# Kernel tuning notes

Hardware: AMD Instinct MI355X
Metric: run time of the kernel (lower is better)

Reference implementation:

```python
import jax, jax.numpy as jnp
import numpy as np

B, N, R, S, FIN, NCLS, KNN = 16, 2048, 64, 64, 6, 40, 40


def _knn_laplacian(x, k):
    # pairwise squared distance -> gaussian affinity -> row-wise top-k sparsify
    # -> symmetric-normalized Laplacian  L = I - D^{-1/2} A D^{-1/2}
    xx = jnp.sum(x * x, axis=-1)                      # [B,N]
    inner = jnp.einsum('bnd,bmd->bnm', x, x)          # [B,N,N]
    dist = xx[:, :, None] + xx[:, None, :] - 2.0 * inner
    A = jnp.exp(-dist)
    kth = jax.lax.top_k(A, k)[0][..., -1]             # k-th largest per row [B,N]
    A = jnp.where(A >= kth[..., None], A, jnp.zeros((), A.dtype))
    d = jnp.sum(A, axis=-1)
    dis = jnp.where(d > 0, jax.lax.rsqrt(jnp.maximum(d, 1e-12)), jnp.zeros((), A.dtype))
    L = jnp.eye(A.shape[-1], dtype=A.dtype) - dis[:, :, None] * A * dis[:, None, :]
    return L


def _cheb_conv(x, L, w, b):
    # DenseChebConv, K=3: T0=x, T1=Lx, T2=2LT1-T0, then linear on concat
    t0 = x
    t1 = jnp.matmul(L, x)
    t2 = 2.0 * jnp.matmul(L, t1) - t0
    xc = jnp.concatenate([t0, t1, t2], axis=-1)       # [B,N,3*Fin]
    return jnp.matmul(xc, w) + b


def setup_inputs() -> dict:
    key = jax.random.key(0)
    ks = jax.random.split(key, 16)
    p = lambda k_, sh: (jax.random.normal(k_, sh, dtype=jnp.float32) * 0.02)
    return {
        'x': jax.random.normal(ks[0], (B, N, FIN), dtype=jnp.float32),
        'laplacian_Reeb': jax.random.normal(ks[1], (B, R, R), dtype=jnp.float32),
        'sccs': jax.random.randint(ks[2], (B, R, S), 0, N),
        'vertices_reeb': jax.random.normal(ks[3], (B * R, 3), dtype=jnp.float32),
        'edges_reeb': jax.random.randint(ks[4], (B, 128, 2), 0, R),
        'labels': jax.random.randint(ks[5], (B,), 0, NCLS),
        'k': KNN, 'batch_size': B, 'num_points': N,
        'conv1_w': p(ks[6], (3 * FIN, 128)), 'conv1_b': jnp.zeros((128,), jnp.float32),
        'conv2_w': p(ks[7], (3 * 128, 512)), 'conv2_b': jnp.zeros((512,), jnp.float32),
        'convReeb_w': p(ks[8], (3 * 128, 512)), 'convReeb_b': jnp.zeros((512,), jnp.float32),
        'fc1_w': p(ks[9], (1024, 512)), 'fc1_b': jnp.zeros((512,), jnp.float32),
        'fc2_w': p(ks[10], (512, 128)), 'fc2_b': jnp.zeros((128,), jnp.float32),
        'fc3_w': p(ks[11], (128, NCLS)), 'fc3_b': jnp.zeros((NCLS,), jnp.float32),
    }


def reference(x, laplacian_Reeb, sccs, vertices_reeb, edges_reeb, labels, k,
              batch_size, num_points, conv1_w, conv1_b, conv2_w, conv2_b,
              convReeb_w, convReeb_b, fc1_w, fc1_b, fc2_w, fc2_b, fc3_w, fc3_b):
    regs = []
    # graph build is under no_grad in the original
    L = jax.lax.stop_gradient(_knn_laplacian(x, k))
    out = jax.nn.relu(_cheb_conv(x, L, conv1_w, conv1_b))           # [B,N,128]
    regs.append(jnp.linalg.norm(jnp.einsum('bnf,bnm,bmg->bfg', out, L, out)) ** 2)

    # Reeb ragged segment-max pool (no_grad in original): gather SCC index
    # groups per Reeb node and max-reduce -> [B,R,128]
    gathered = jax.vmap(lambda o, s: o[s])(out, sccs)               # [B,R,S,128]
    Vertices_final_Reeb = jax.lax.stop_gradient(jnp.max(gathered, axis=2))
    laplacian_Reeb_final = jax.lax.stop_gradient(laplacian_Reeb)

    L2 = jax.lax.stop_gradient(_knn_laplacian(out, k))
    out = jax.nn.relu(_cheb_conv(out, L2, conv2_w, conv2_b))        # [B,N,512]
    regs.append(jnp.linalg.norm(jnp.einsum('bnf,bnm,bmg->bfg', out, L2, out)) ** 2)

    out_Reeb = jax.nn.relu(_cheb_conv(Vertices_final_Reeb, laplacian_Reeb_final,
                                      convReeb_w, convReeb_b))      # [B,R,512]
    regs.append(jnp.linalg.norm(jnp.einsum('brf,brq,bqg->bfg', out_Reeb,
                                           laplacian_Reeb_final, out_Reeb)) ** 2)

    out = jnp.max(out, axis=1)            # [B,512]
    out_Reeb = jnp.max(out_Reeb, axis=1)  # [B,512]
    out = jnp.concatenate([out_Reeb, out], axis=1)                  # [B,1024]

    out = jnp.matmul(out, fc1_w) + fc1_b
    regs.append(jnp.linalg.norm(fc1_w[:, 0]) ** 2); regs.append(fc1_b[0] ** 2)
    out = jax.nn.relu(out)
    out = jnp.matmul(out, fc2_w) + fc2_b
    regs.append(jnp.linalg.norm(fc2_w[:, 0]) ** 2); regs.append(fc2_b[0] ** 2)
    out = jax.nn.relu(out)
    out = jnp.matmul(out, fc3_w) + fc3_b
    regs.append(jnp.linalg.norm(fc3_w[:, 0]) ** 2); regs.append(fc3_b[0] ** 2)
    return out, jnp.stack(regs)
```

## Files before the change

### kernel.cpp

```cpp
#include <hip/hip_runtime.h>

#define NB 16
#define NP 2048
#define NR 64
#define NS 64
#define KSEL 40

typedef __attribute__((ext_vector_type(8))) short bf16x8;
typedef __attribute__((ext_vector_type(4))) float f32x4;

constexpr long aOUT1 = 0;
constexpr long aT1A  = aOUT1 + 16L*2048*128;
constexpr long aT2A  = aT1A  + 16L*2048*6;
constexpr long aZ1   = aT2A  + 16L*2048*6;
constexpr long aM1   = aZ1   + 16L*2048*128;
constexpr long aVALS1= aM1   + 16L*128*128;
constexpr long aDIS1 = aVALS1+ 16L*2048*64;
constexpr long aVALS2= aDIS1 + 16L*2048;
constexpr long aDIS2 = aVALS2+ 16L*2048*64;
constexpr long aXX2  = aDIS2 + 16L*2048;
constexpr long aXX1  = aXX2  + 16L*2048;
constexpr long aG4   = aXX1  + 16L*2048;
constexpr long aT1B  = aG4   + 4L*2048*2048;
constexpr long aT2B  = aT1B  + 16L*2048*128;
constexpr long aOUT2 = aT2B  + 16L*2048*128;
constexpr long aZ2   = aOUT2 + 16L*2048*512;
constexpr long aM2   = aZ2   + 16L*2048*512;
constexpr long aVFR  = aM2   + 16L*512*512;
constexpr long aT1R  = aVFR  + 16L*64*128;
constexpr long aT2R  = aT1R  + 16L*64*128;
constexpr long aOUTR = aT2R  + 16L*64*128;
constexpr long aZR   = aOUTR + 16L*64*512;
constexpr long aMR   = aZR   + 16L*64*512;
constexpr long aPOOL = aMR   + 16L*512*512;
constexpr long aFC1O = aPOOL + 16L*1024;
constexpr long aFC2O = aFC1O + 16L*512;
constexpr long aMPP  = aFC2O + 16L*128;
constexpr long FTOT  = aMPP  + 16L*8*512;

constexpr long iCOLS1 = 0;
constexpr long iCNT1  = iCOLS1 + 16L*2048*64;
constexpr long iCOLS2 = iCNT1  + 16L*2048;
constexpr long iCNT2  = iCOLS2 + 16L*2048*64;
constexpr long ITOT   = iCNT2  + 16L*2048;

constexpr long uOUT1H = 0;
constexpr long uOUT1L = uOUT1H + 16L*2048*128;
constexpr long uT1BH  = uOUT1L + 16L*2048*128;
constexpr long uT1BL  = uT1BH  + 16L*2048*128;
constexpr long uT2BH  = uT1BL  + 16L*2048*128;
constexpr long uT2BL  = uT2BH  + 16L*2048*128;
constexpr long uW2TH  = uT2BL  + 16L*2048*128;
constexpr long uW2TL  = uW2TH  + 512L*384;
constexpr long uVFRH  = uW2TL  + 512L*384;
constexpr long uVFRL  = uVFRH  + 16L*64*128;
constexpr long uT1RH  = uVFRL  + 16L*64*128;
constexpr long uT1RL  = uT1RH  + 16L*64*128;
constexpr long uT2RH  = uT1RL  + 16L*64*128;
constexpr long uT2RL  = uT2RH  + 16L*64*128;
constexpr long uWRTH  = uT2RL  + 16L*64*128;
constexpr long uWRTL  = uWRTH  + 512L*384;
constexpr long uOUT1T = uWRTL  + 512L*384;
constexpr long uZ1T   = uOUT1T + 16L*128*2048;
constexpr long uOUT2T = uZ1T   + 16L*128*2048;
constexpr long uZ2T   = uOUT2T + 16L*512*2048;
constexpr long uOUTRT = uZ2T   + 16L*512*2048;
constexpr long uZRT   = uOUTRT + 16L*512*64;
constexpr long uOUT2B = uZRT   + 16L*512*64;
constexpr long UTOT   = uOUT2B + 16L*2048*512;

__device__ __align__(256) float  g_farena[FTOT];
__device__ __align__(256) int    g_iarena[ITOT];
__device__ __align__(256) ushort g_uarena[UTOT];

__device__ __forceinline__ float wsum_f(float v){
  #pragma unroll
  for (int s=32;s>0;s>>=1) v += __shfl_xor(v, s, 64);
  return v;
}
__device__ __forceinline__ int wsum_i(int v){
  #pragma unroll
  for (int s=32;s>0;s>>=1) v += __shfl_xor(v, s, 64);
  return v;
}

__device__ __forceinline__ void gl2lds16(const void* g, void* l){
  __builtin_amdgcn_global_load_lds(
      (const __attribute__((address_space(1))) void*)g,
      (__attribute__((address_space(3))) void*)l, 16, 0, 0);
}

__device__ __forceinline__ unsigned fkey(float f){
  unsigned b = __float_as_uint(f);
  return b ^ (((unsigned)((int)b >> 31)) | 0x80000000u);
}
__device__ __forceinline__ float fkey_inv(unsigned k){
  unsigned m = ((unsigned)((int)(~k) >> 31)) | 0x80000000u;
  return __uint_as_float(k ^ m);
}

__device__ __forceinline__ void topk_store(unsigned (&uk)[32], int lane, long row,
    int* __restrict__ cols, float* __restrict__ vals,
    int* __restrict__ cnt, float* __restrict__ dis)
{
  unsigned kmax = uk[0], kmin = uk[0];
  #pragma unroll
  for (int q=1;q<32;++q){
    kmax = kmax > uk[q] ? kmax : uk[q];
    kmin = kmin < uk[q] ? kmin : uk[q];
  }
  #pragma unroll
  for (int s=32;s>0;s>>=1){
    unsigned o1 = (unsigned)__shfl_xor((int)kmax, s, 64);
    unsigned o2 = (unsigned)__shfl_xor((int)kmin, s, 64);
    kmax = kmax > o1 ? kmax : o1;
    kmin = kmin < o2 ? kmin : o2;
  }
  unsigned lo = kmin, hi = kmax + 1u;
  int cLo = 2048, cHi = 0, it = 0;
  while (cLo != KSEL && hi - lo > 1u){
    unsigned t;
    if (it & 1){
      t = lo + ((hi - lo) >> 1);
    } else {
      float flo = fkey_inv(lo), fhi = fkey_inv(hi);
      float ft = flo + (fhi - flo) * ((float)(cLo - KSEL) / (float)(cLo - cHi));
      t = fkey(ft);
      if (t <= lo) t = lo + 1u;
      else if (t >= hi) t = hi - 1u;
    }
    ++it;
    int c = 0;
    #pragma unroll
    for (int q=0;q<32;++q) c += (int)__popcll(__ballot(uk[q] >= t));
    if (c >= KSEL){ lo = t; cLo = c; } else { hi = t; cHi = c; }
  }
  unsigned kth = lo;
  int kc = 0;
  #pragma unroll
  for (int q=0;q<32;++q) kc += (uk[q] >= kth) ? 1 : 0;
  int tot = wsum_i(kc);
  int incl = kc;
  #pragma unroll
  for (int s=1;s<64;s<<=1){ int u = __shfl_up(incl, s, 64); if (lane >= s) incl += u; }
  int pos = incl - kc;
  int* cp = cols + row*64; float* vp = vals + row*64;
  float d = 0.f;
  #pragma unroll
  for (int q=0;q<32;++q){
    if (uk[q] >= kth){
      float v = __expf(fkey_inv(uk[q]));
      d += v;
      if (pos < 64){ cp[pos] = q*64 + lane; vp[pos] = v; }
      pos++;
    }
  }
  d = wsum_f(d);
  if (lane == 0){
    cnt[row] = tot <= 64 ? tot : 64;
    dis[row] = d > 0.f ? (1.0f / sqrtf(fmaxf(d, 1e-12f))) : 0.f;
  }
}

__global__ __launch_bounds__(256) void xx6_kernel(const float* __restrict__ x,
    float* __restrict__ xx1)
{
  long i = (long)blockIdx.x*256 + threadIdx.x;
  const float* p = x + i*6;
  float2 v0 = *(const float2*)(p);
  float2 v1 = *(const float2*)(p+2);
  float2 v2 = *(const float2*)(p+4);
  xx1[i] = v0.x*v0.x + v0.y*v0.y + v1.x*v1.x + v1.y*v1.y + v2.x*v2.x + v2.y*v2.y;
}

__global__ __launch_bounds__(256) void knn1_kernel(const float* __restrict__ x,
    const float* __restrict__ xx1,
    int* __restrict__ cols, float* __restrict__ vals, int* __restrict__ cnt,
    float* __restrict__ dis)
{
  int lane = threadIdx.x & 63;
  long row = (long)blockIdx.x*4 + (threadIdx.x >> 6);
  int b = (int)(row >> 11); int i = (int)(row & (NP-1));
  const float* xb = x + (long)b*NP*6;
  const float* xxb = xx1 + ((long)b << 11);
  float xi[6];
  #pragma unroll
  for (int d2=0; d2<6; ++d2) xi[d2] = xb[(long)i*6 + d2];
  float xxi = xxb[i];
  unsigned uk[32];
  #pragma unroll 4
  for (int c=0;c<32;++c){
    int j = c*64 + lane;
    const float* xj = xb + (long)j*6;
    float2 v0 = *(const float2*)(xj);
    float2 v1 = *(const float2*)(xj+2);
    float2 v2 = *(const float2*)(xj+4);
    float inr = xi[0]*v0.x + xi[1]*v0.y + xi[2]*v1.x + xi[3]*v1.y + xi[4]*v2.x + xi[5]*v2.y;
    uk[c] = fkey(2.f*inr - xxi - xxb[j]);
  }
  topk_store(uk, lane, row, cols, vals, cnt, dis);
}

__global__ __launch_bounds__(256) void knn2_kernel(const float* __restrict__ G,
    const float* __restrict__ xx, int batch0,
    int* __restrict__ cols, float* __restrict__ vals, int* __restrict__ cnt,
    float* __restrict__ dis)
{
  int lane = threadIdx.x & 63;
  long lrow = (long)blockIdx.x*4 + (threadIdx.x >> 6);
  int lb = (int)(lrow >> 11); int i = (int)(lrow & (NP-1));
  long row = ((long)(batch0+lb) << 11) + i;
  const float* Gr = G + ((long)lb*NP + i)*NP;
  const float* xxb = xx + ((long)(batch0+lb) << 11);
  float xxi = xxb[i];
  unsigned uk[32];
  #pragma unroll 4
  for (int c=0;c<32;++c){
    int j = c*64 + lane;
    uk[c] = fkey(2.f*Gr[j] - xxi - xxb[j]);
  }
  topk_store(uk, lane, row, cols, vals, cnt, dis);
}

__global__ __launch_bounds__(256) void spmm6_kernel(const float* __restrict__ X,
    const float* __restrict__ T0, float* __restrict__ Y,
    const int* __restrict__ cols, const float* __restrict__ vals,
    const int* __restrict__ cnt, const float* __restrict__ dis,
    float c1, float c2, float cs)
{
  long row = (long)blockIdx.x*256 + threadIdx.x;
  int b = (int)(row >> 11);
  const float* Xb = X + ((long)b << 11)*6;
  const float* db = dis + ((long)b << 11);
  float acc[6] = {0,0,0,0,0,0};
  int c = cnt[row];
  const int* cp = cols + row*64; const float* vp = vals + row*64;
  for (int t=0;t<c;++t){
    int j = cp[t];
    float w = vp[t] * db[j];
    const float* xr = Xb + (long)j*6;
    #pragma unroll
    for (int d2=0; d2<6; ++d2) acc[d2] += w * xr[d2];
  }
  float di = dis[row];
  #pragma unroll
  for (int d2=0; d2<6; ++d2)
    Y[row*6+d2] = c1*X[row*6+d2] + c2*T0[row*6+d2] - cs*di*acc[d2];
}

template<int W>
__global__ __launch_bounds__((W >= 256) ? 256 : W) void spmm_kernel(
    const float* __restrict__ X, const float* __restrict__ T0, float* __restrict__ Y,
    const int* __restrict__ cols, const float* __restrict__ vals,
    const int* __restrict__ cnt, const float* __restrict__ dis,
    float c1, float c2, float cs)
{
  constexpr int TPB = (W >= 256) ? 256 : W;
  constexpr int E = W / TPB;
  __shared__ int scol[64];
  __shared__ float sval[64];
  int q = blockIdx.x;
  long row = ((long)(q & 7) << 12) + (q >> 3);
  int b = (int)(row >> 11);
  int tid = threadIdx.x;
  int c = cnt[row];
  if (tid < 64){ scol[tid] = cols[row*64+tid]; sval[tid] = vals[row*64+tid]; }
  __syncthreads();
  const float* Xb = X + ((long)b << 11)*W;
  const float* db = dis + ((long)b << 11);
  float acc[E] = {};
  for (int t=0;t<c;++t){
    int j = scol[t];
    float w = sval[t] * db[j];
    const float* xr = Xb + (long)j*W;
    #pragma unroll
    for (int e=0;e<E;++e) acc[e] += w * xr[tid + e*TPB];
  }
  float di = dis[row];
  #pragma unroll
  for (int e=0;e<E;++e){
    long idx = row*W + tid + e*TPB;
    Y[idx] = c1*X[idx] + c2*T0[idx] - cs*di*acc[e];
  }
}

__global__ __launch_bounds__(256) void spmmb_kernel(
    const float* __restrict__ X, const ushort* __restrict__ Xb,
    float* __restrict__ Y,
    const int* __restrict__ cols, const float* __restrict__ vals,
    const int* __restrict__ cnt, const float* __restrict__ dis)
{
  __shared__ int scol[4][64];
  __shared__ float sval[4][64];
  int q = blockIdx.x;
  int wid = threadIdx.x >> 6, lane = threadIdx.x & 63;
  long row = ((long)(q & 7) << 12) + ((long)(q >> 3) << 2) + wid;
  int b = (int)(row >> 11);
  scol[wid][lane] = cols[row*64 + lane];
  sval[wid][lane] = vals[row*64 + lane];
  const ushort* Xbb = Xb + ((long)b << 11)*512;
  const float* db = dis + ((long)b << 11);
  int c = cnt[row];
  float acc[8] = {};
  for (int t=0;t<c;++t){
    int j = scol[wid][t];
    float w = sval[wid][t] * db[j];
    bf16x8 v = *(const bf16x8*)(Xbb + (long)j*512 + lane*8);
    #pragma unroll
    for (int e=0;e<8;++e)
      acc[e] += w * __uint_as_float(((unsigned)(ushort)v[e]) << 16);
  }
  float di = dis[row];
  long base = row*512 + lane*8;
  float4 x0 = *(const float4*)(X + base);
  float4 x1 = *(const float4*)(X + base + 4);
  float4 o0, o1;
  o0.x = x0.x - di*acc[0]; o0.y = x0.y - di*acc[1];
  o0.z = x0.z - di*acc[2]; o0.w = x0.w - di*acc[3];
  o1.x = x1.x - di*acc[4]; o1.y = x1.y - di*acc[5];
  o1.z = x1.z - di*acc[6]; o1.w = x1.w - di*acc[7];
  *(float4*)(Y + base) = o0;
  *(float4*)(Y + base + 4) = o1;
}

__global__ __launch_bounds__(128) void conv1_kernel(const float* __restrict__ x,
    const float* __restrict__ t1, const float* __restrict__ t2,
    const float* __restrict__ w, const float* __restrict__ bias,
    float* __restrict__ out)
{
  long row = blockIdx.x; int o = threadIdx.x;
  float acc = bias[o];
  const float* xr = x + row*6; const float* a1 = t1 + row*6; const float* a2 = t2 + row*6;
  #pragma unroll
  for (int d2=0; d2<6; ++d2){
    acc += xr[d2]*w[d2*128 + o];
    acc += a1[d2]*w[(6+d2)*128 + o];
    acc += a2[d2]*w[(12+d2)*128 + o];
  }
  out[row*128 + o] = fmaxf(acc, 0.f);
}

__global__ __launch_bounds__(256) void pack_hilo_kernel(const float* __restrict__ X,
    ushort* __restrict__ H, ushort* __restrict__ L, long n4)
{
  long i = (long)blockIdx.x*256 + threadIdx.x;
  if (i >= n4) return;
  float4 v = *(const float4*)(X + i*4);
  float xs[4] = {v.x, v.y, v.z, v.w};
  ushort h[4], l[4];
  #pragma unroll
  for (int q=0;q<4;++q){
    unsigned u = __float_as_uint(xs[q]);
    h[q] = (ushort)(u >> 16);
    float hf = __uint_as_float(u & 0xffff0000u);
    float r = xs[q] - hf;
    l[q] = (ushort)(__float_as_uint(r) >> 16);
  }
  *(ushort4*)(H + i*4) = make_ushort4(h[0],h[1],h[2],h[3]);
  *(ushort4*)(L + i*4) = make_ushort4(l[0],l[1],l[2],l[3]);
}

__global__ __launch_bounds__(256) void pack_rne_kernel(const float* __restrict__ X,
    ushort* __restrict__ H, long n4)
{
  long i = (long)blockIdx.x*256 + threadIdx.x;
  if (i >= n4) return;
  float4 v = *(const float4*)(X + i*4);
  float xs[4] = {v.x, v.y, v.z, v.w};
  ushort h[4];
  #pragma unroll
  for (int q=0;q<4;++q){
    unsigned u = __float_as_uint(xs[q]);
    u += 0x7fffu + ((u >> 16) & 1u);
    h[q] = (ushort)(u >> 16);
  }
  *(ushort4*)(H + i*4) = make_ushort4(h[0],h[1],h[2],h[3]);
}

template<bool HILO>
__global__ __launch_bounds__(256) void tpack_kernel(const float* __restrict__ X,
    ushort* __restrict__ H, ushort* __restrict__ L,
    int R, int C, long sIn, long sOut)
{
  __shared__ float tile[32][33];
  int c0 = blockIdx.x*32, r0 = blockIdx.y*32, b = blockIdx.z;
  const float* Xb = X + (long)b*sIn;
  int tx = threadIdx.x & 31, ty = threadIdx.x >> 5;
  #pragma unroll
  for (int rr=ty; rr<32; rr+=8)
    tile[rr][tx] = Xb[(long)(r0+rr)*C + c0+tx];
  __syncthreads();
  #pragma unroll
  for (int cc=ty; cc<32; cc+=8){
    float xv = tile[tx][cc];
    long oidx = (long)b*sOut + (long)(c0+cc)*R + r0 + tx;
    unsigned u = __float_as_uint(xv);
    if (HILO){
      H[oidx] = (ushort)(u >> 16);
      float hf = __uint_as_float(u & 0xffff0000u);
      float r = xv - hf;
      L[oidx] = (ushort)(__float_as_uint(r) >> 16);
    } else {
      u += 0x7fffu + ((u >> 16) & 1u);
      H[oidx] = (ushort)(u >> 16);
    }
  }
}

__global__ __launch_bounds__(256) void mirror_kernel(float* __restrict__ G)
{
  int p = blockIdx.y;
  int t = p, bx = 0, rem = 15;
  while (t >= rem){ t -= rem; --rem; ++bx; }
  int by = bx + 1 + t;
  int sub = blockIdx.x;
  int si = sub >> 2, sj = sub & 3;
  int r0 = bx*128 + si*32;
  int c0 = by*128 + sj*32;
  float* Gb = G + (long)blockIdx.z*NP*NP;
  __shared__ float tile[32][33];
  int tx = threadIdx.x & 31, ty = threadIdx.x >> 5;
  #pragma unroll
  for (int rr=ty; rr<32; rr+=8)
    tile[rr][tx] = Gb[(long)(r0+rr)*NP + c0+tx];
  __syncthreads();
  #pragma unroll
  for (int rr=ty; rr<32; rr+=8)
    Gb[(long)(c0+rr)*NP + r0+tx] = tile[tx][rr];
}

template<bool SPLIT, bool CHEB, bool BR, bool TRI>
__global__ __launch_bounds__(256) void mgemm_kernel(
    const ushort* __restrict__ Ah0, const ushort* __restrict__ Ah1, const ushort* __restrict__ Ah2,
    const ushort* __restrict__ Al0, const ushort* __restrict__ Al1, const ushort* __restrict__ Al2,
    const ushort* __restrict__ Bh, const ushort* __restrict__ Bl,
    const float* __restrict__ bias, float* __restrict__ C,
    int M, int N, int K, long sA, long sB, long sC)
{
  __shared__ ushort AsH[128*32];
  __shared__ ushort BsH[128*32];
  __shared__ ushort AsL[SPLIT ? 128*32 : 8];
  __shared__ ushort BsL[SPLIT ? 128*32 : 8];
  int bz = blockIdx.z;
  int m0, n0;
  if constexpr (TRI){
    int t = blockIdx.x, bx = 0, rem = 16;
    while (t >= rem){ t -= rem; --rem; ++bx; }
    m0 = bx*128; n0 = (bx + t)*128;
  } else {
    m0 = blockIdx.x*128; n0 = blockIdx.y*128;
  }
  int tid = threadIdx.x, lane = tid & 63, wid = tid >> 6;
  int wm = (wid & 1)*64, wn = (wid >> 1)*64;
  f32x4 acc[4][4] = {};
  const ushort* Bb  = Bh + (long)bz*sB;
  const ushort* Blb = SPLIT ? (Bl + (long)bz*sB) : (const ushort*)nullptr;
  const ushort* Ab  = CHEB ? Ah0 : (Ah0 + (long)bz*sA);
  const ushort* Alb = (SPLIT && !CHEB) ? (Al0 + (long)bz*sA) : Al0;

  for (int k0 = 0; k0 < K; k0 += 32){
    #pragma unroll
    for (int cc2=0; cc2<2; ++cc2){
      int chunk = wid*2 + cc2;
      int e = chunk*512 + lane*8;
      int row = e >> 5;
      int slot = (e >> 3) & 3;
      int scol = (slot ^ ((row >> 1) & 3)) * 8;
      const ushort* asrc;
      if (CHEB){
        int kg2 = k0 + scol;
        const ushort* base = (kg2 < 128) ? Ah0 : ((kg2 < 256) ? Ah1 : Ah2);
        asrc = base + (long)(m0+row)*128 + (kg2 & 127);
      } else {
        asrc = Ab + (long)(m0+row)*K + k0 + scol;
      }
      gl2lds16(asrc, &AsH[chunk*512]);
      gl2lds16(Bb + (long)(n0+row)*K + k0 + scol, &BsH[chunk*512]);
      if (SPLIT){
        const ushort* alsrc;
        if (CHEB){
          int kg2 = k0 + scol;
          const ushort* base = (kg2 < 128) ? Al0 : ((kg2 < 256) ? Al1 : Al2);
          alsrc = base + (long)(m0+row)*128 + (kg2 & 127);
        } else {
          alsrc = Alb + (long)(m0+row)*K + k0 + scol;
        }
        gl2lds16(alsrc, &AsL[chunk*512]);
        gl2lds16(Blb + (long)(n0+row)*K + k0 + scol, &BsL[chunk*512]);
      }
    }
    __syncthreads();
    int lr = lane & 15, kg = lane >> 4;
    bf16x8 af[4], bfr[4];
    #pragma unroll
    for (int f=0; f<4; ++f){
      int ra = wm + f*16 + lr;
      int rb = wn + f*16 + lr;
      af[f]  = *(const bf16x8*)&AsH[ra*32 + (kg ^ ((ra>>1)&3))*8];
      bfr[f] = *(const bf16x8*)&BsH[rb*32 + (kg ^ ((rb>>1)&3))*8];
    }
    if (SPLIT){
      bf16x8 al[4], bl[4];
      #pragma unroll
      for (int f=0; f<4; ++f){
        int ra = wm + f*16 + lr;
        int rb = wn + f*16 + lr;
        al[f] = *(const bf16x8*)&AsL[ra*32 + (kg ^ ((ra>>1)&3))*8];
        bl[f] = *(const bf16x8*)&BsL[rb*32 + (kg ^ ((rb>>1)&3))*8];
      }
      #pragma unroll
      for (int mf=0; mf<4; ++mf)
        #pragma unroll
        for (int nf=0; nf<4; ++nf){
          acc[mf][nf] = __builtin_amdgcn_mfma_f32_16x16x32_bf16(af[mf], bfr[nf], acc[mf][nf], 0,0,0);
          acc[mf][nf] = __builtin_amdgcn_mfma_f32_16x16x32_bf16(af[mf], bl[nf],  acc[mf][nf], 0,0,0);
          acc[mf][nf] = __builtin_amdgcn_mfma_f32_16x16x32_bf16(al[mf], bfr[nf], acc[mf][nf], 0,0,0);
        }
    } else {
      #pragma unroll
      for (int mf=0; mf<4; ++mf)
        #pragma unroll
        for (int nf=0; nf<4; ++nf)
          acc[mf][nf] = __builtin_amdgcn_mfma_f32_16x16x32_bf16(af[mf], bfr[nf], acc[mf][nf], 0,0,0);
    }
    __syncthreads();
  }
  int lr = lane & 15, l4 = (lane >> 4)*4;
  #pragma unroll
  for (int mf=0; mf<4; ++mf){
    #pragma unroll
    for (int nf=0; nf<4; ++nf){
      int n = n0 + wn + nf*16 + lr;
      float bv = BR ? bias[n] : 0.f;
      #pragma unroll
      for (int r=0; r<4; ++r){
        int m = m0 + wm + mf*16 + l4 + r;
        float v = acc[mf][nf][r];
        if (BR) v = fmaxf(v + bv, 0.f);
        C[(long)bz*sC + (long)m*N + n] = v;
      }
    }
  }
}

__global__ __launch_bounds__(256) void rownorm_kernel(const float* __restrict__ X,
    float* __restrict__ xx)
{
  int lane = threadIdx.x & 63;
  long row = (long)blockIdx.x*4 + (threadIdx.x >> 6);
  const float* p = X + row*128;
  float v0 = p[lane], v1 = p[64+lane];
  float s = wsum_f(v0*v0 + v1*v1);
  if (lane == 0) xx[row] = s;
}

__global__ __launch_bounds__(128) void reeb_pool_kernel(const float* __restrict__ out1,
    const int* __restrict__ sccs, float* __restrict__ VfR)
{
  int q = blockIdx.x;
  int br = ((q & 7) << 7) + (q >> 3);
  int b = br >> 6;
  int f = threadIdx.x;
  const int* sp = sccs + (long)br*NS;
  const float* ob = out1 + ((long)b << 11)*128;
  float m = -1e30f;
  for (int s=0;s<NS;++s){
    int idx = sp[s];
    m = fmaxf(m, ob[(long)idx*128 + f]);
  }
  VfR[(long)br*128 + f] = m;
}

template<int W>
__global__ __launch_bounds__((W>=256)?256:W) void reeb_mm_kernel(const float* __restrict__ L,
    const float* __restrict__ X, const float* __restrict__ T0, float* __restrict__ Y,
    float cs, float c2)
{
  constexpr int TPB = (W>=256)?256:W;
  constexpr int E = W/TPB;
  int br = blockIdx.x; int b = br >> 6; int r = br & 63;
  const float* lr = L + ((long)b*NR + r)*NR;
  const float* Xb = X + (long)b*NR*W;
  int tid = threadIdx.x;
  float acc[E] = {};
  for (int q=0;q<NR;++q){
    float w = lr[q];
    #pragma unroll
    for (int e=0;e<E;++e) acc[e] += w * Xb[(long)q*W + tid + e*TPB];
  }
  #pragma unroll
  for (int e=0;e<E;++e){
    long idx = (long)br*W + tid + e*TPB;
    Y[idx] = cs*acc[e] + c2*T0[idx];
  }
}

__global__ __launch_bounds__(512) void maxpool1_kernel(const float* __restrict__ X,
    float* __restrict__ part)
{
  int b = blockIdx.x, rc = blockIdx.y; int f = threadIdx.x;
  const float* p = X + ((long)b*2048 + (long)rc*256)*512 + f;
  float m = -1e30f;
  #pragma unroll 4
  for (int r=0;r<256;++r) m = fmaxf(m, p[(long)r*512]);
  part[((long)b*8+rc)*512 + f] = m;
}

__global__ __launch_bounds__(512) void maxpool2_kernel(const float* __restrict__ part,
    const float* __restrict__ outR, float* __restrict__ pool)
{
  int b = blockIdx.x; int f = threadIdx.x;
  const float* pp = part + (long)b*8*512 + f;
  float m = -1e30f;
  #pragma unroll
  for (int r=0;r<8;++r) m = fmaxf(m, pp[r*512]);
  pool[(long)b*1024 + 512 + f] = m;
  const float* rp = outR + (long)b*64*512 + f;
  float mr = -1e30f;
  #pragma unroll 4
  for (int r=0;r<64;++r) mr = fmaxf(mr, rp[(long)r*512]);
  pool[(long)b*1024 + f] = mr;
}

template<bool RELU>
__global__ __launch_bounds__(256) void fc_kernel(const float* __restrict__ in,
    const float* __restrict__ W, const float* __restrict__ bias,
    float* __restrict__ out, int IN, int OUT)
{
  __shared__ float red[4][64];
  int b = blockIdx.x, o0 = blockIdx.y*64;
  int tid = threadIdx.x;
  int ol = tid & 63, q = tid >> 6;
  int o = o0 + ol;
  const float* ip = in + (long)b*IN;
  float acc = 0.f;
  if (o < OUT){
    int kb = IN >> 2;
    int ks = q*kb;
    for (int i=0;i<kb;i+=8){
      #pragma unroll
      for (int u=0;u<8;++u){
        int k = ks + i + u;
        acc += ip[k]*W[(long)k*OUT + o];
      }
    }
  }
  red[q][ol] = acc;
  __syncthreads();
  if (tid < 64){
    int oo = o0 + tid;
    if (oo < OUT){
      float s = red[0][tid]+red[1][tid]+red[2][tid]+red[3][tid] + bias[oo];
      out[(long)b*OUT + oo] = RELU ? fmaxf(s, 0.f) : s;
    }
  }
}

__global__ __launch_bounds__(256) void sumsq_kernel(const float* __restrict__ X, int n,
    float* __restrict__ tgt)
{
  __shared__ float ps[4];
  int tid = threadIdx.x; int lane = tid & 63, wid = tid >> 6;
  float s = 0.f;
  for (long i = (long)blockIdx.x*256 + tid; i < n; i += (long)gridDim.x*256){
    float v = X[i]; s += v*v;
  }
  s = wsum_f(s);
  if (lane == 0) ps[wid] = s;
  __syncthreads();
  if (tid == 0) atomicAdd(tgt, ps[0]+ps[1]+ps[2]+ps[3]);
}

__global__ __launch_bounds__(256) void wreg_kernel(const float* __restrict__ w1,
    const float* __restrict__ b1, const float* __restrict__ w2, const float* __restrict__ b2,
    const float* __restrict__ w3, const float* __restrict__ b3, float* __restrict__ out9)
{
  __shared__ float ps[3][4];
  int tid = threadIdx.x, lane = tid & 63, wid = tid >> 6;
  float s1 = 0.f, s2 = 0.f, s3 = 0.f;
  for (int i=tid;i<1024;i+=256){ float v = w1[(long)i*512]; s1 += v*v; }
  for (int i=tid;i<512;i+=256){ float v = w2[(long)i*128]; s2 += v*v; }
  if (tid < 128){ float v = w3[(long)tid*40]; s3 = v*v; }
  s1 = wsum_f(s1); s2 = wsum_f(s2); s3 = wsum_f(s3);
  if (lane == 0){ ps[0][wid]=s1; ps[1][wid]=s2; ps[2][wid]=s3; }
  __syncthreads();
  if (tid == 0){
    out9[3] = ps[0][0]+ps[0][1]+ps[0][2]+ps[0][3];
    out9[4] = b1[0]*b1[0];
    out9[5] = ps[1][0]+ps[1][1]+ps[1][2]+ps[1][3];
    out9[6] = b2[0]*b2[0];
    out9[7] = ps[2][0]+ps[2][1]+ps[2][2]+ps[2][3];
    out9[8] = b3[0]*b3[0];
  }
}

extern "C" void kernel_launch(void* const* d_in, const int* in_sizes, int n_in,
                              void* d_out, int out_size, void* d_ws, size_t ws_size,
                              hipStream_t stream)
{
  (void)in_sizes; (void)n_in; (void)d_ws; (void)ws_size; (void)out_size;
  const float* x    = (const float*)d_in[0];
  const float* lapR = (const float*)d_in[1];
  const int*   sccs = (const int*)d_in[2];
  const float* w1   = (const float*)d_in[9];
  const float* b1   = (const float*)d_in[10];
  const float* w2   = (const float*)d_in[11];
  const float* b2   = (const float*)d_in[12];
  const float* wR   = (const float*)d_in[13];
  const float* bRb  = (const float*)d_in[14];
  const float* fw1  = (const float*)d_in[15];
  const float* fb1  = (const float*)d_in[16];
  const float* fw2  = (const float*)d_in[17];
  const float* fb2  = (const float*)d_in[18];
  const float* fw3  = (const float*)d_in[19];
  const float* fb3  = (const float*)d_in[20];
  float* out = (float*)d_out;

  float* Fb = nullptr; int* Ib = nullptr; ushort* Ub = nullptr;
  hipGetSymbolAddress((void**)&Fb, HIP_SYMBOL(g_farena));
  hipGetSymbolAddress((void**)&Ib, HIP_SYMBOL(g_iarena));
  hipGetSymbolAddress((void**)&Ub, HIP_SYMBOL(g_uarena));

  float* out1 = Fb + aOUT1;  float* t1a = Fb + aT1A;  float* t2a = Fb + aT2A;
  float* Z1   = Fb + aZ1;    float* M1  = Fb + aM1;
  float* vals1= Fb + aVALS1; float* dis1= Fb + aDIS1;
  float* vals2= Fb + aVALS2; float* dis2= Fb + aDIS2;
  float* xx2  = Fb + aXX2;   float* xx1 = Fb + aXX1;  float* G4  = Fb + aG4;
  float* t1b  = Fb + aT1B;   float* t2b = Fb + aT2B;
  float* out2 = Fb + aOUT2;  float* Z2  = Fb + aZ2;   float* M2 = Fb + aM2;
  float* VfR  = Fb + aVFR;   float* t1R = Fb + aT1R;  float* t2R= Fb + aT2R;
  float* outR = Fb + aOUTR;  float* ZR  = Fb + aZR;   float* MR = Fb + aMR;
  float* pool = Fb + aPOOL;  float* fc1o= Fb + aFC1O; float* fc2o=Fb + aFC2O;
  float* mpp  = Fb + aMPP;
  int* cols1 = Ib + iCOLS1; int* cnt1 = Ib + iCNT1;
  int* cols2 = Ib + iCOLS2; int* cnt2 = Ib + iCNT2;
  ushort* out1h = Ub + uOUT1H; ushort* out1l = Ub + uOUT1L;
  ushort* t1bh  = Ub + uT1BH;  ushort* t1bl  = Ub + uT1BL;
  ushort* t2bh  = Ub + uT2BH;  ushort* t2bl  = Ub + uT2BL;
  ushort* w2th  = Ub + uW2TH;  ushort* w2tl  = Ub + uW2TL;
  ushort* vfrh  = Ub + uVFRH;  ushort* vfrl  = Ub + uVFRL;
  ushort* t1rh  = Ub + uT1RH;  ushort* t1rl  = Ub + uT1RL;
  ushort* t2rh  = Ub + uT2RH;  ushort* t2rl  = Ub + uT2RL;
  ushort* wrth  = Ub + uWRTH;  ushort* wrtl  = Ub + uWRTL;
  ushort* out1t = Ub + uOUT1T; ushort* z1t   = Ub + uZ1T;
  ushort* out2t = Ub + uOUT2T; ushort* z2t   = Ub + uZ2T;
  ushort* outrt = Ub + uOUTRT; ushort* zrt   = Ub + uZRT;
  ushort* out2b = Ub + uOUT2B;

  hipMemsetAsync(out + 640, 0, 9*sizeof(float), stream);

  xx6_kernel<<<dim3(128),dim3(256),0,stream>>>(x, xx1);
  knn1_kernel<<<dim3(8192),dim3(256),0,stream>>>(x, xx1, cols1, vals1, cnt1, dis1);
  spmm6_kernel<<<dim3(128),dim3(256),0,stream>>>(x, x, t1a, cols1, vals1, cnt1, dis1, 1.f, 0.f, 1.f);
  spmm6_kernel<<<dim3(128),dim3(256),0,stream>>>(t1a, x, t2a, cols1, vals1, cnt1, dis1, 2.f, -1.f, 2.f);
  conv1_kernel<<<dim3(32768),dim3(128),0,stream>>>(x, t1a, t2a, w1, b1, out1);
  pack_hilo_kernel<<<dim3(4096),dim3(256),0,stream>>>(out1, out1h, out1l, 16L*2048*128/4);

  spmm_kernel<128><<<dim3(32768),dim3(128),0,stream>>>(out1, out1, Z1, cols1, vals1, cnt1, dis1, 1.f, 0.f, 1.f);
  tpack_kernel<false><<<dim3(4,64,16),dim3(256),0,stream>>>(out1, out1t, nullptr, 2048,128, 2048L*128, 128L*2048);
  tpack_kernel<false><<<dim3(4,64,16),dim3(256),0,stream>>>(Z1,   z1t,   nullptr, 2048,128, 2048L*128, 128L*2048);
  mgemm_kernel<false,false,false,false><<<dim3(1,1,16),dim3(256),0,stream>>>(
      out1t,nullptr,nullptr, nullptr,nullptr,nullptr, z1t,nullptr, nullptr, M1,
      128,128,2048, 128L*2048, 128L*2048, 128L*128);
  sumsq_kernel<<<dim3(512),dim3(256),0,stream>>>(M1, 16*128*128, out+640);
  reeb_pool_kernel<<<dim3(1024),dim3(128),0,stream>>>(out1, sccs, VfR);

  rownorm_kernel<<<dim3(8192),dim3(256),0,stream>>>(out1, xx2);
  for (int g=0; g<4; ++g){
    long off = (long)g*4*NP*128;
    mgemm_kernel<true,false,false,true><<<dim3(136,1,4),dim3(256),0,stream>>>(
        out1h+off,nullptr,nullptr, out1l+off,nullptr,nullptr, out1h+off, out1l+off, nullptr, G4,
        2048,2048,128, (long)NP*128, (long)NP*128, (long)NP*NP);
    mirror_kernel<<<dim3(16,120,4),dim3(256),0,stream>>>(G4);
    knn2_kernel<<<dim3(2048),dim3(256),0,stream>>>(G4, xx2, g*4, cols2, vals2, cnt2, dis2);
  }
  spmm_kernel<128><<<dim3(32768),dim3(128),0,stream>>>(out1, out1, t1b, cols2, vals2, cnt2, dis2, 1.f, 0.f, 1.f);
  spmm_kernel<128><<<dim3(32768),dim3(128),0,stream>>>(t1b, out1, t2b, cols2, vals2, cnt2, dis2, 2.f, -1.f, 2.f);
  pack_hilo_kernel<<<dim3(4096),dim3(256),0,stream>>>(t1b, t1bh, t1bl, 16L*2048*128/4);
  pack_hilo_kernel<<<dim3(4096),dim3(256),0,stream>>>(t2b, t2bh, t2bl, 16L*2048*128/4);
  tpack_kernel<true><<<dim3(16,12,1),dim3(256),0,stream>>>(w2, w2th, w2tl, 384,512, 0,0);
  mgemm_kernel<true,true,true,false><<<dim3(256,4,1),dim3(256),0,stream>>>(
      out1h,t1bh,t2bh, out1l,t1bl,t2bl, w2th, w2tl, b2, out2,
      32768,512,384, 0,0,0);
  pack_rne_kernel<<<dim3(16384),dim3(256),0,stream>>>(out2, out2b, 16L*2048*512/4);
  spmmb_kernel<<<dim3(8192),dim3(256),0,stream>>>(out2, out2b, Z2, cols2, vals2, cnt2, dis2);
  tpack_kernel<false><<<dim3(16,64,16),dim3(256),0,stream>>>(out2, out2t, nullptr, 2048,512, 2048L*512, 512L*2048);
  tpack_kernel<false><<<dim3(16,64,16),dim3(256),0,stream>>>(Z2,   z2t,   nullptr, 2048,512, 2048L*512, 512L*2048);
  mgemm_kernel<false,false,false,false><<<dim3(4,4,16),dim3(256),0,stream>>>(
      out2t,nullptr,nullptr, nullptr,nullptr,nullptr, z2t,nullptr, nullptr, M2,
      512,512,2048, 512L*2048, 512L*2048, 512L*512);
  sumsq_kernel<<<dim3(512),dim3(256),0,stream>>>(M2, 16*512*512, out+641);

  reeb_mm_kernel<128><<<dim3(1024),dim3(128),0,stream>>>(lapR, VfR, VfR, t1R, 1.f, 0.f);
  reeb_mm_kernel<128><<<dim3(1024),dim3(128),0,stream>>>(lapR, t1R, VfR, t2R, 2.f, -1.f);
  pack_hilo_kernel<<<dim3(128),dim3(256),0,stream>>>(VfR, vfrh, vfrl, 16L*64*128/4);
  pack_hilo_kernel<<<dim3(128),dim3(256),0,stream>>>(t1R, t1rh, t1rl, 16L*64*128/4);
  pack_hilo_kernel<<<dim3(128),dim3(256),0,stream>>>(t2R, t2rh, t2rl, 16L*64*128/4);
  tpack_kernel<true><<<dim3(16,12,1),dim3(256),0,stream>>>(wR, wrth, wrtl, 384,512, 0,0);
  mgemm_kernel<true,true,true,false><<<dim3(8,4,1),dim3(256),0,stream>>>(
      vfrh,t1rh,t2rh, vfrl,t1rl,t2rl, wrth, wrtl, bRb, outR,
      1024,512,384, 0,0,0);
  reeb_mm_kernel<512><<<dim3(1024),dim3(256),0,stream>>>(lapR, outR, outR, ZR, 1.f, 0.f);
  tpack_kernel<false><<<dim3(16,2,16),dim3(256),0,stream>>>(outR, outrt, nullptr, 64,512, 64L*512, 512L*64);
  tpack_kernel<false><<<dim3(16,2,16),dim3(256),0,stream>>>(ZR,   zrt,   nullptr, 64,512, 64L*512, 512L*64);
  mgemm_kernel<false,false,false,false><<<dim3(4,4,16),dim3(256),0,stream>>>(
      outrt,nullptr,nullptr, nullptr,nullptr,nullptr, zrt,nullptr, nullptr, MR,
      512,512,64, 512L*64, 512L*64, 512L*512);
  sumsq_kernel<<<dim3(512),dim3(256),0,stream>>>(MR, 16*512*512, out+642);

  maxpool1_kernel<<<dim3(16,8),dim3(512),0,stream>>>(out2, mpp);
  maxpool2_kernel<<<dim3(16),dim3(512),0,stream>>>(mpp, outR, pool);
  fc_kernel<true ><<<dim3(16,8),dim3(256),0,stream>>>(pool, fw1, fb1, fc1o, 1024, 512);
  fc_kernel<true ><<<dim3(16,2),dim3(256),0,stream>>>(fc1o, fw2, fb2, fc2o, 512, 128);
  fc_kernel<false><<<dim3(16,1),dim3(256),0,stream>>>(fc2o, fw3, fb3, out, 128, 40);
  wreg_kernel<<<dim3(1),dim3(256),0,stream>>>(fw1, fb1, fw2, fb2, fw3, fb3, out+640);
}
```

Baseline: 1.216 ms.

## Fuse bf16 packing, Gram mirroring and sum-of-squares into producer kernels

```diff
diff --git a/kernel.cpp b/kernel.cpp
--- a/kernel.cpp
+++ b/kernel.cpp
@@ -25,14 +25,12 @@
 constexpr long aT2B  = aT1B  + 16L*2048*128;
 constexpr long aOUT2 = aT2B  + 16L*2048*128;
 constexpr long aZ2   = aOUT2 + 16L*2048*512;
-constexpr long aM2   = aZ2   + 16L*2048*512;
-constexpr long aVFR  = aM2   + 16L*512*512;
+constexpr long aVFR  = aZ2   + 16L*2048*512;
 constexpr long aT1R  = aVFR  + 16L*64*128;
 constexpr long aT2R  = aT1R  + 16L*64*128;
 constexpr long aOUTR = aT2R  + 16L*64*128;
 constexpr long aZR   = aOUTR + 16L*64*512;
-constexpr long aMR   = aZR   + 16L*64*512;
-constexpr long aPOOL = aMR   + 16L*512*512;
+constexpr long aPOOL = aZR   + 16L*64*512;
 constexpr long aFC1O = aPOOL + 16L*1024;
 constexpr long aFC2O = aFC1O + 16L*512;
 constexpr long aMPP  = aFC2O + 16L*128;
@@ -46,7 +44,8 @@
 
 constexpr long uOUT1H = 0;
 constexpr long uOUT1L = uOUT1H + 16L*2048*128;
-constexpr long uT1BH  = uOUT1L + 16L*2048*128;
+constexpr long uOUT1R = uOUT1L + 16L*2048*128;
+constexpr long uT1BH  = uOUT1R + 16L*2048*128;
 constexpr long uT1BL  = uT1BH  + 16L*2048*128;
 constexpr long uT2BH  = uT1BL  + 16L*2048*128;
 constexpr long uT2BL  = uT2BH  + 16L*2048*128;
@@ -90,6 +89,18 @@
       (__attribute__((address_space(3))) void*)l, 16, 0, 0);
 }
 
+__device__ __forceinline__ ushort bf_rne(float x){
+  unsigned u = __float_as_uint(x);
+  u += 0x7fffu + ((u >> 16) & 1u);
+  return (ushort)(u >> 16);
+}
+__device__ __forceinline__ void bf_hilo(float x, ushort& h, ushort& l){
+  unsigned u = __float_as_uint(x);
+  h = (ushort)(u >> 16);
+  float hf = __uint_as_float(u & 0xffff0000u);
+  l = (ushort)(__float_as_uint(x - hf) >> 16);
+}
+
 __device__ __forceinline__ unsigned fkey(float f){
   unsigned b = __float_as_uint(f);
   return b ^ (((unsigned)((int)b >> 31)) | 0x80000000u);
@@ -248,9 +259,10 @@
     Y[row*6+d2] = c1*X[row*6+d2] + c2*T0[row*6+d2] - cs*di*acc[d2];
 }
 
-template<int W>
+template<int W, bool PACK>
 __global__ __launch_bounds__((W >= 256) ? 256 : W) void spmm_kernel(
     const float* __restrict__ X, const float* __restrict__ T0, float* __restrict__ Y,
+    ushort* __restrict__ Hh, ushort* __restrict__ Ll,
     const int* __restrict__ cols, const float* __restrict__ vals,
     const int* __restrict__ cnt, const float* __restrict__ dis,
     float c1, float c2, float cs)
@@ -280,7 +292,12 @@
   #pragma unroll
   for (int e=0;e<E;++e){
     long idx = row*W + tid + e*TPB;
-    Y[idx] = c1*X[idx] + c2*T0[idx] - cs*di*acc[e];
+    float y = c1*X[idx] + c2*T0[idx] - cs*di*acc[e];
+    Y[idx] = y;
+    if (PACK){
+      ushort h, l; bf_hilo(y, h, l);
+      Hh[idx] = h; Ll[idx] = l;
+    }
   }
 }
 
@@ -326,7 +343,8 @@
 __global__ __launch_bounds__(128) void conv1_kernel(const float* __restrict__ x,
     const float* __restrict__ t1, const float* __restrict__ t2,
     const float* __restrict__ w, const float* __restrict__ bias,
-    float* __restrict__ out)
+    float* __restrict__ out, ushort* __restrict__ oh, ushort* __restrict__ ol,
+    ushort* __restrict__ orr)
 {
   long row = blockIdx.x; int o = threadIdx.x;
   float acc = bias[o];
@@ -337,44 +355,12 @@
     acc += a1[d2]*w[(6+d2)*128 + o];
     acc += a2[d2]*w[(12+d2)*128 + o];
   }
-  out[row*128 + o] = fmaxf(acc, 0.f);
-}
-
-__global__ __launch_bounds__(256) void pack_hilo_kernel(const float* __restrict__ X,
-    ushort* __restrict__ H, ushort* __restrict__ L, long n4)
-{
-  long i = (long)blockIdx.x*256 + threadIdx.x;
-  if (i >= n4) return;
-  float4 v = *(const float4*)(X + i*4);
-  float xs[4] = {v.x, v.y, v.z, v.w};
-  ushort h[4], l[4];
-  #pragma unroll
-  for (int q=0;q<4;++q){
-    unsigned u = __float_as_uint(xs[q]);
-    h[q] = (ushort)(u >> 16);
-    float hf = __uint_as_float(u & 0xffff0000u);
-    float r = xs[q] - hf;
-    l[q] = (ushort)(__float_as_uint(r) >> 16);
-  }
-  *(ushort4*)(H + i*4) = make_ushort4(h[0],h[1],h[2],h[3]);
-  *(ushort4*)(L + i*4) = make_ushort4(l[0],l[1],l[2],l[3]);
-}
-
-__global__ __launch_bounds__(256) void pack_rne_kernel(const float* __restrict__ X,
-    ushort* __restrict__ H, long n4)
-{
-  long i = (long)blockIdx.x*256 + threadIdx.x;
-  if (i >= n4) return;
-  float4 v = *(const float4*)(X + i*4);
-  float xs[4] = {v.x, v.y, v.z, v.w};
-  ushort h[4];
-  #pragma unroll
-  for (int q=0;q<4;++q){
-    unsigned u = __float_as_uint(xs[q]);
-    u += 0x7fffu + ((u >> 16) & 1u);
-    h[q] = (ushort)(u >> 16);
-  }
-  *(ushort4*)(H + i*4) = make_ushort4(h[0],h[1],h[2],h[3]);
+  acc = fmaxf(acc, 0.f);
+  long idx = row*128 + o;
+  out[idx] = acc;
+  ushort h, l; bf_hilo(acc, h, l);
+  oh[idx] = h; ol[idx] = l;
+  orr[idx] = bf_rne(acc);
 }
 
 template<bool HILO>
@@ -394,39 +380,13 @@
   for (int cc=ty; cc<32; cc+=8){
     float xv = tile[tx][cc];
     long oidx = (long)b*sOut + (long)(c0+cc)*R + r0 + tx;
-    unsigned u = __float_as_uint(xv);
     if (HILO){
-      H[oidx] = (ushort)(u >> 16);
-      float hf = __uint_as_float(u & 0xffff0000u);
-      float r = xv - hf;
-      L[oidx] = (ushort)(__float_as_uint(r) >> 16);
+      ushort h, l; bf_hilo(xv, h, l);
+      H[oidx] = h; L[oidx] = l;
     } else {
-      u += 0x7fffu + ((u >> 16) & 1u);
-      H[oidx] = (ushort)(u >> 16);
-    }
-  }
-}
-
-__global__ __launch_bounds__(256) void mirror_kernel(float* __restrict__ G)
-{
-  int p = blockIdx.y;
-  int t = p, bx = 0, rem = 15;
-  while (t >= rem){ t -= rem; --rem; ++bx; }
-  int by = bx + 1 + t;
-  int sub = blockIdx.x;
-  int si = sub >> 2, sj = sub & 3;
-  int r0 = bx*128 + si*32;
-  int c0 = by*128 + sj*32;
-  float* Gb = G + (long)blockIdx.z*NP*NP;
-  __shared__ float tile[32][33];
-  int tx = threadIdx.x & 31, ty = threadIdx.x >> 5;
-  #pragma unroll
-  for (int rr=ty; rr<32; rr+=8)
-    tile[rr][tx] = Gb[(long)(r0+rr)*NP + c0+tx];
-  __syncthreads();
-  #pragma unroll
-  for (int rr=ty; rr<32; rr+=8)
-    Gb[(long)(c0+rr)*NP + r0+tx] = tile[tx][rr];
+      H[oidx] = bf_rne(xv);
+    }
+  }
 }
 
 template<bool SPLIT, bool CHEB, bool BR, bool TRI>
@@ -435,6 +395,7 @@
     const ushort* __restrict__ Al0, const ushort* __restrict__ Al1, const ushort* __restrict__ Al2,
     const ushort* __restrict__ Bh, const ushort* __restrict__ Bl,
     const float* __restrict__ bias, float* __restrict__ C,
+    ushort* __restrict__ Cb, float* __restrict__ ssq,
     int M, int N, int K, long sA, long sB, long sC)
 {
   __shared__ ushort AsH[128*32];
@@ -526,6 +487,18 @@
     __syncthreads();
   }
   int lr = lane & 15, l4 = (lane >> 4)*4;
+  if (ssq){
+    float s = 0.f;
+    #pragma unroll
+    for (int mf=0; mf<4; ++mf)
+      #pragma unroll
+      for (int nf=0; nf<4; ++nf)
+        #pragma unroll
+        for (int r=0; r<4; ++r){ float v = acc[mf][nf][r]; s += v*v; }
+    s = wsum_f(s);
+    if (lane == 0) atomicAdd(ssq, s);
+    return;
+  }
   #pragma unroll
   for (int mf=0; mf<4; ++mf){
     #pragma unroll
@@ -538,6 +511,8 @@
         float v = acc[mf][nf][r];
         if (BR) v = fmaxf(v + bv, 0.f);
         C[(long)bz*sC + (long)m*N + n] = v;
+        if (TRI) C[(long)bz*sC + (long)n*N + m] = v;
+        if (Cb) Cb[(long)bz*sC + (long)m*N + n] = bf_rne(v);
       }
     }
   }
@@ -555,7 +530,8 @@
 }
 
 __global__ __launch_bounds__(128) void reeb_pool_kernel(const float* __restrict__ out1,
-    const int* __restrict__ sccs, float* __restrict__ VfR)
+    const int* __restrict__ sccs, float* __restrict__ VfR,
+    ushort* __restrict__ Hh, ushort* __restrict__ Ll)
 {
   int q = blockIdx.x;
   int br = ((q & 7) << 7) + (q >> 3);
@@ -568,18 +544,22 @@
     int idx = sp[s];
     m = fmaxf(m, ob[(long)idx*128 + f]);
   }
-  VfR[(long)br*128 + f] = m;
-}
-
-template<int W>
-__global__ __launch_bounds__((W>=256)?256:W) void reeb_mm_kernel(const float* __restrict__ L,
+  long oidx = (long)br*128 + f;
+  VfR[oidx] = m;
+  ushort h, l; bf_hilo(m, h, l);
+  Hh[oidx] = h; Ll[oidx] = l;
+}
+
+template<int W, bool PACK>
+__global__ __launch_bounds__((W>=256)?256:W) void reeb_mm_kernel(const float* __restrict__ Lap,
     const float* __restrict__ X, const float* __restrict__ T0, float* __restrict__ Y,
+    ushort* __restrict__ Hh, ushort* __restrict__ Ll,
     float cs, float c2)
 {
   constexpr int TPB = (W>=256)?256:W;
   constexpr int E = W/TPB;
   int br = blockIdx.x; int b = br >> 6; int r = br & 63;
-  const float* lr = L + ((long)b*NR + r)*NR;
+  const float* lr = Lap + ((long)b*NR + r)*NR;
   const float* Xb = X + (long)b*NR*W;
   int tid = threadIdx.x;
   float acc[E] = {};
@@ -591,7 +571,12 @@
   #pragma unroll
   for (int e=0;e<E;++e){
     long idx = (long)br*W + tid + e*TPB;
-    Y[idx] = cs*acc[e] + c2*T0[idx];
+    float y = cs*acc[e] + c2*T0[idx];
+    Y[idx] = y;
+    if (PACK){
+      ushort h, l; bf_hilo(y, h, l);
+      Hh[idx] = h; Ll[idx] = l;
+    }
   }
 }
 
@@ -654,21 +639,6 @@
       out[(long)b*OUT + oo] = RELU ? fmaxf(s, 0.f) : s;
     }
   }
-}
-
-__global__ __launch_bounds__(256) void sumsq_kernel(const float* __restrict__ X, int n,
-    float* __restrict__ tgt)
-{
-  __shared__ float ps[4];
-  int tid = threadIdx.x; int lane = tid & 63, wid = tid >> 6;
-  float s = 0.f;
-  for (long i = (long)blockIdx.x*256 + tid; i < n; i += (long)gridDim.x*256){
-    float v = X[i]; s += v*v;
-  }
-  s = wsum_f(s);
-  if (lane == 0) ps[wid] = s;
-  __syncthreads();
-  if (tid == 0) atomicAdd(tgt, ps[0]+ps[1]+ps[2]+ps[3]);
 }
 
 __global__ __launch_bounds__(256) void wreg_kernel(const float* __restrict__ w1,
@@ -727,14 +697,16 @@
   float* vals2= Fb + aVALS2; float* dis2= Fb + aDIS2;
   float* xx2  = Fb + aXX2;   float* xx1 = Fb + aXX1;  float* G4  = Fb + aG4;
   float* t1b  = Fb + aT1B;   float* t2b = Fb + aT2B;
-  float* out2 = Fb + aOUT2;  float* Z2  = Fb + aZ2;   float* M2 = Fb + aM2;
+  float* out2 = Fb + aOUT2;  float* Z2  = Fb + aZ2;
   float* VfR  = Fb + aVFR;   float* t1R = Fb + aT1R;  float* t2R= Fb + aT2R;
-  float* outR = Fb + aOUTR;  float* ZR  = Fb + aZR;   float* MR = Fb + aMR;
+  float* outR = Fb + aOUTR;  float* ZR  = Fb + aZR;
   float* pool = Fb + aPOOL;  float* fc1o= Fb + aFC1O; float* fc2o=Fb + aFC2O;
   float* mpp  = Fb + aMPP;
+  (void)M1;
   int* cols1 = Ib + iCOLS1; int* cnt1 = Ib + iCNT1;
   int* cols2 = Ib + iCOLS2; int* cnt2 = Ib + iCNT2;
   ushort* out1h = Ub + uOUT1H; ushort* out1l = Ub + uOUT1L;
+  ushort* out1r = Ub + uOUT1R;
   ushort* t1bh  = Ub + uT1BH;  ushort* t1bl  = Ub + uT1BL;
   ushort* t2bh  = Ub + uT2BH;  ushort* t2bl  = Ub + uT2BL;
   ushort* w2th  = Ub + uW2TH;  ushort* w2tl  = Ub + uW2TL;
@@ -753,60 +725,52 @@
   knn1_kernel<<<dim3(8192),dim3(256),0,stream>>>(x, xx1, cols1, vals1, cnt1, dis1);
   spmm6_kernel<<<dim3(128),dim3(256),0,stream>>>(x, x, t1a, cols1, vals1, cnt1, dis1, 1.f, 0.f, 1.f);
   spmm6_kernel<<<dim3(128),dim3(256),0,stream>>>(t1a, x, t2a, cols1, vals1, cnt1, dis1, 2.f, -1.f, 2.f);
-  conv1_kernel<<<dim3(32768),dim3(128),0,stream>>>(x, t1a, t2a, w1, b1, out1);
-  pack_hilo_kernel<<<dim3(4096),dim3(256),0,stream>>>(out1, out1h, out1l, 16L*2048*128/4);
-
-  spmm_kernel<128><<<dim3(32768),dim3(128),0,stream>>>(out1, out1, Z1, cols1, vals1, cnt1, dis1, 1.f, 0.f, 1.f);
+  conv1_kernel<<<dim3(32768),dim3(128),0,stream>>>(x, t1a, t2a, w1, b1, out1, out1h, out1l, out1r);
+
+  spmm_kernel<128,false><<<dim3(32768),dim3(128),0,stream>>>(out1, out1, Z1, nullptr, nullptr,
+      cols1, vals1, cnt1, dis1, 1.f, 0.f, 1.f);
   tpack_kernel<false><<<dim3(4,64,16),dim3(256),0,stream>>>(out1, out1t, nullptr, 2048,128, 2048L*128, 128L*2048);
   tpack_kernel<false><<<dim3(4,64,16),dim3(256),0,stream>>>(Z1,   z1t,   nullptr, 2048,128, 2048L*128, 128L*2048);
   mgemm_kernel<false,false,false,false><<<dim3(1,1,16),dim3(256),0,stream>>>(
-      out1t,nullptr,nullptr, nullptr,nullptr,nullptr, z1t,nullptr, nullptr, M1,
-      128,128,2048, 128L*2048, 128L*2048, 128L*128);
-  sumsq_kernel<<<dim3(512),dim3(256),0,stream>>>(M1, 16*128*128, out+640);
-  reeb_pool_kernel<<<dim3(1024),dim3(128),0,stream>>>(out1, sccs, VfR);
+      out1t,nullptr,nullptr, nullptr,nullptr,nullptr, z1t,nullptr, nullptr, nullptr,
+      nullptr, out+640, 128,128,2048, 128L*2048, 128L*2048, 0);
+  reeb_pool_kernel<<<dim3(1024),dim3(128),0,stream>>>(out1, sccs, VfR, vfrh, vfrl);
 
   rownorm_kernel<<<dim3(8192),dim3(256),0,stream>>>(out1, xx2);
   for (int g=0; g<4; ++g){
     long off = (long)g*4*NP*128;
-    mgemm_kernel<true,false,false,true><<<dim3(136,1,4),dim3(256),0,stream>>>(
-        out1h+off,nullptr,nullptr, out1l+off,nullptr,nullptr, out1h+off, out1l+off, nullptr, G4,
-        2048,2048,128, (long)NP*128, (long)NP*128, (long)NP*NP);
-    mirror_kernel<<<dim3(16,120,4),dim3(256),0,stream>>>(G4);
+    mgemm_kernel<false,false,false,true><<<dim3(136,1,4),dim3(256),0,stream>>>(
+        out1r+off,nullptr,nullptr, nullptr,nullptr,nullptr, out1r+off, nullptr, nullptr, G4,
+        nullptr, nullptr, 2048,2048,128, (long)NP*128, (long)NP*128, (long)NP*NP);
     knn2_kernel<<<dim3(2048),dim3(256),0,stream>>>(G4, xx2, g*4, cols2, vals2, cnt2, dis2);
   }
-  spmm_kernel<128><<<dim3(32768),dim3(128),0,stream>>>(out1, out1, t1b, cols2, vals2, cnt2, dis2, 1.f, 0.f, 1.f);
-  spmm_kernel<128><<<dim3(32768),dim3(128),0,stream>>>(t1b, out1, t2b, cols2, vals2, cnt2, dis2, 2.f, -1.f, 2.f);
-  pack_hilo_kernel<<<dim3(4096),dim3(256),0,stream>>>(t1b, t1bh, t1bl, 16L*2048*128/4);
-  pack_hilo_kernel<<<dim3(4096),dim3(256),0,stream>>>(t2b, t2bh, t2bl, 16L*2048*128/4);
+  spmm_kernel<128,true><<<dim3(32768),dim3(128),0,stream>>>(out1, out1, t1b, t1bh, t1bl,
+      cols2, vals2, cnt2, dis2, 1.f, 0.f, 1.f);
+  spmm_kernel<128,true><<<dim3(32768),dim3(128),0,stream>>>(t1b, out1, t2b, t2bh, t2bl,
+      cols2, vals2, cnt2, dis2, 2.f, -1.f, 2.f);
   tpack_kernel<true><<<dim3(16,12,1),dim3(256),0,stream>>>(w2, w2th, w2tl, 384,512, 0,0);
   mgemm_kernel<true,true,true,false><<<dim3(256,4,1),dim3(256),0,stream>>>(
       out1h,t1bh,t2bh, out1l,t1bl,t2bl, w2th, w2tl, b2, out2,
-      32768,512,384, 0,0,0);
-  pack_rne_kernel<<<dim3(16384),dim3(256),0,stream>>>(out2, out2b, 16L*2048*512/4);
+      out2b, nullptr, 32768,512,384, 0,0,0);
   spmmb_kernel<<<dim3(8192),dim3(256),0,stream>>>(out2, out2b, Z2, cols2, vals2, cnt2, dis2);
   tpack_kernel<false><<<dim3(16,64,16),dim3(256),0,stream>>>(out2, out2t, nullptr, 2048,512, 2048L*512, 512L*2048);
   tpack_kernel<false><<<dim3(16,64,16),dim3(256),0,stream>>>(Z2,   z2t,   nullptr, 2048,512, 2048L*512, 512L*2048);
   mgemm_kernel<false,false,false,false><<<dim3(4,4,16),dim3(256),0,stream>>>(
-      out2t,nullptr,nullptr, nullptr,nullptr,nullptr, z2t,nullptr, nullptr, M2,
-      512,512,2048, 512L*2048, 512L*2048, 512L*512);
-  sumsq_kernel<<<dim3(512),dim3(256),0,stream>>>(M2, 16*512*512, out+641);
-
-  reeb_mm_kernel<128><<<dim3(1024),dim3(128),0,stream>>>(lapR, VfR, VfR, t1R, 1.f, 0.f);
-  reeb_mm_kernel<128><<<dim3(1024),dim3(128),0,stream>>>(lapR, t1R, VfR, t2R, 2.f, -1.f);
-  pack_hilo_kernel<<<dim3(128),dim3(256),0,stream>>>(VfR, vfrh, vfrl, 16L*64*128/4);
-  pack_hilo_kernel<<<dim3(128),dim3(256),0,stream>>>(t1R, t1rh, t1rl, 16L*64*128/4);
-  pack_hilo_kernel<<<dim3(128),dim3(256),0,stream>>>(t2R, t2rh, t2rl, 16L*64*128/4);
+      out2t,nullptr,nullptr, nullptr,nullptr,nullptr, z2t,nullptr, nullptr, nullptr,
+      nullptr, out+641, 512,512,2048, 512L*2048, 512L*2048, 0);
+
+  reeb_mm_kernel<128,true><<<dim3(1024),dim3(128),0,stream>>>(lapR, VfR, VfR, t1R, t1rh, t1rl, 1.f, 0.f);
+  reeb_mm_kernel<128,true><<<dim3(1024),dim3(128),0,stream>>>(lapR, t1R, VfR, t2R, t2rh, t2rl, 2.f, -1.f);
   tpack_kernel<true><<<dim3(16,12,1),dim3(256),0,stream>>>(wR, wrth, wrtl, 384,512, 0,0);
   mgemm_kernel<true,true,true,false><<<dim3(8,4,1),dim3(256),0,stream>>>(
       vfrh,t1rh,t2rh, vfrl,t1rl,t2rl, wrth, wrtl, bRb, outR,
-      1024,512,384, 0,0,0);
-  reeb_mm_kernel<512><<<dim3(1024),dim3(256),0,stream>>>(lapR, outR, outR, ZR, 1.f, 0.f);
+      nullptr, nullptr, 1024,512,384, 0,0,0);
+  reeb_mm_kernel<512,false><<<dim3(1024),dim3(256),0,stream>>>(lapR, outR, outR, ZR, nullptr, nullptr, 1.f, 0.f);
   tpack_kernel<false><<<dim3(16,2,16),dim3(256),0,stream>>>(outR, outrt, nullptr, 64,512, 64L*512, 512L*64);
   tpack_kernel<false><<<dim3(16,2,16),dim3(256),0,stream>>>(ZR,   zrt,   nullptr, 64,512, 64L*512, 512L*64);
   mgemm_kernel<false,false,false,false><<<dim3(4,4,16),dim3(256),0,stream>>>(
-      outrt,nullptr,nullptr, nullptr,nullptr,nullptr, zrt,nullptr, nullptr, MR,
-      512,512,64, 512L*64, 512L*64, 512L*512);
-  sumsq_kernel<<<dim3(512),dim3(256),0,stream>>>(MR, 16*512*512, out+642);
+      outrt,nullptr,nullptr, nullptr,nullptr,nullptr, zrt,nullptr, nullptr, nullptr,
+      nullptr, out+642, 512,512,64, 512L*64, 512L*64, 0);
 
   maxpool1_kernel<<<dim3(16,8),dim3(512),0,stream>>>(out2, mpp);
   maxpool2_kernel<<<dim3(16),dim3(512),0,stream>>>(mpp, outR, pool);
```

Result: no change. 1.207 ms (-0.7%).
